# Optimization experiments

Measured on AMD Instinct MI355X. Metric: run time of the kernel, lower is better.

The kernel has to match this reference:

```python
import jax, jax.numpy as jnp
import numpy as np
from jax import lax

B, T, N, D = 8, 64, 197, 768
HID = 4
K_FRAME, K_TOKEN = 8, 49
LAMBDA_COV, LAMBDA_SCORE = 1.0, 0.5
LN_EPS = 1e-5


def setup_inputs() -> dict:
    key = jax.random.key(0)
    k = jax.random.split(key, 5)
    x = jax.random.normal(k[0], (B, T, N, D), jnp.float32)
    mask = jax.random.uniform(k[1], (B, T, N), jnp.float32)
    ln_gamma = jnp.ones((D,), jnp.float32)
    ln_beta = jnp.zeros((D,), jnp.float32)
    W1 = jax.random.normal(k[2], (D, HID * D), jnp.float32) * 0.02
    b1 = jnp.zeros((HID * D,), jnp.float32)
    W2 = jax.random.normal(k[3], (HID * D, 1), jnp.float32) * 0.02
    b2 = jnp.zeros((1,), jnp.float32)
    return {"x": x, "mask": mask, "ln_gamma": ln_gamma, "ln_beta": ln_beta,
            "W1": W1, "b1": b1, "W2": W2, "b2": b2}


def _facility_location(frame_repr, score, valid, k):
    # cosine similarity between frames (F.normalize eps = 1e-12)
    fn = frame_repr / jnp.clip(jnp.linalg.norm(frame_repr, axis=-1, keepdims=True), 1e-12)
    sim = jnp.einsum('bid,bjd->bij', fn, fn)  # [B,T,T]
    Bb, Tt = score.shape

    def step(carry, _):
        best_cover, chosen = carry  # [B,T], [B,T] bool
        # coverage gain per candidate j: sum_i max(best[i], sim[i,j]) - best[i]
        cov_gain = jnp.maximum(best_cover[:, :, None], sim).sum(1) - best_cover.sum(1, keepdims=True)
        total = LAMBDA_COV * cov_gain + LAMBDA_SCORE * score
        total = jnp.where(valid & (~chosen), total, -jnp.inf)
        j = jnp.argmax(total, axis=1)  # [B]
        sim_j = jnp.take_along_axis(sim, j[:, None, None], axis=2)[..., 0]  # [B,T]
        best_cover = jnp.maximum(best_cover, sim_j)
        chosen = chosen.at[jnp.arange(Bb), j].set(True)
        return (best_cover, chosen), j

    init = (jnp.zeros((Bb, Tt), frame_repr.dtype), jnp.zeros((Bb, Tt), bool))
    (_, chosen), js = lax.scan(step, init, None, length=k)
    return js.T, chosen.astype(frame_repr.dtype)  # frame_idx [B,k], frame_mask [B,T]


def _kcenter(X, valid, k):
    # X [N,D], valid [N] bool; greedy k-center (farthest point sampling)
    d0 = jnp.where(valid, (X * X).sum(-1), -jnp.inf)
    first = jnp.argmax(d0)

    def dist_to(i):
        diff = X - X[i]
        return jnp.sqrt((diff * diff).sum(-1))

    min_dist = jnp.where(valid, dist_to(first), -1.0)

    def step(md, _):
        cand = jnp.argmax(md)
        md = jnp.where(valid, jnp.minimum(md, dist_to(cand)), -1.0)
        return md, cand

    _, rest = lax.scan(step, min_dist, None, length=k - 1)
    return jnp.concatenate([first[None], rest])


def _forward(x, mask, ln_gamma, ln_beta, W1, b1, W2, b2):
    # masked mean frame representation (use_cls=False path)
    denom = jnp.clip(mask.sum(2), 1e-6)                      # [B,T]
    frame_repr = (x * mask[..., None]).sum(2) / denom[..., None]  # [B,T,D]
    valid_frame = denom > 0

    # score head: LayerNorm -> Linear -> GELU(exact) -> Linear
    mu = frame_repr.mean(-1, keepdims=True)
    var = ((frame_repr - mu) ** 2).mean(-1, keepdims=True)
    h = (frame_repr - mu) / jnp.sqrt(var + LN_EPS) * ln_gamma + ln_beta
    h = jax.nn.gelu(h @ W1 + b1, approximate=False)
    score = (h @ W2 + b2)[..., 0]                            # [B,T]

    # selection is index-valued: no gradient flows through it (as in torch)
    frame_idx, frame_mask = _facility_location(
        lax.stop_gradient(frame_repr), lax.stop_gradient(score), valid_frame, K_FRAME)

    Xf = jnp.take_along_axis(x, frame_idx[:, :, None, None], axis=1)   # [B,K,N,D]
    mf = jnp.take_along_axis(mask, frame_idx[:, :, None], axis=1) > 0.5  # [B,K,N]

    token_idx = jax.vmap(jax.vmap(lambda Xs, vs: _kcenter(Xs, vs, K_TOKEN)))(
        lax.stop_gradient(Xf), mf)                           # [B,K,Kt]

    b_ar = jnp.arange(x.shape[0])
    token_mask = jnp.zeros(mask.shape, x.dtype).at[
        b_ar[:, None, None], frame_idx[:, :, None], token_idx].set(1.0)

    z = jnp.take_along_axis(Xf, token_idx[..., None], axis=2)  # [B,K,Kt,D]
    return z, frame_idx, token_idx, frame_mask, token_mask


def reference(x, mask, ln_gamma, ln_beta, W1, b1, W2, b2):
    return _forward(x, mask, ln_gamma, ln_beta, W1, b1, W2, b2)
```

## Files before the change

### kernel.cpp

```cpp
#include <hip/hip_runtime.h>
#include <math.h>

#define B_ 8
#define T_ 64
#define N_ 197
#define D_ 768
#define HIDD_ 3072
#define KF_ 8
#define KT_ 49
#define GSTRIDE 200

#define Z_SZ    (B_*KF_*KT_*D_)
#define FI_OFF  (Z_SZ)
#define TI_OFF  (FI_OFF + B_*KF_)
#define FM_OFF  (TI_OFF + B_*KF_*KT_)
#define TM_OFF  (FM_OFF + B_*T_)
#define TM_SZ   (B_*T_*N_)

#define WS_SCOREP  0
#define WS_FN64    98304
#define WS_H32     (WS_FN64 + 3145728)
#define WS_VALID   (WS_H32 + 1572864)
#define WS_FIDX    (WS_VALID + 2048)
#define WS_SIM     (WS_FIDX + 256)
#define WS_G       (WS_SIM + 262144)

__global__ __launch_bounds__(256) void kA(const float* __restrict__ x,
                                          const float* __restrict__ mask,
                                          const float* __restrict__ gamma,
                                          const float* __restrict__ beta,
                                          double* __restrict__ fn64,
                                          float* __restrict__ h32,
                                          int* __restrict__ validw) {
  const int row = blockIdx.x;
  const int tid = threadIdx.x;
  __shared__ float  ms[N_];
  __shared__ double red[256];
  __shared__ double sh_denom, sh_mu, sh_sd, sh_nrm;
  const float* xr = x + (size_t)row * (N_ * D_);

  if (tid < N_) ms[tid] = mask[(size_t)row * N_ + tid];
  __syncthreads();

  red[tid] = (tid < N_) ? (double)ms[tid] : 0.0;
  __syncthreads();
  for (int s = 128; s > 0; s >>= 1) { if (tid < s) red[tid] += red[tid + s]; __syncthreads(); }
  if (tid == 0) { double d = red[0]; sh_denom = (d > 1e-6) ? d : 1e-6; }
  __syncthreads();
  const double dn = sh_denom;

  double a0 = 0.0, a1 = 0.0, a2 = 0.0, a3 = 0.0;
  if (tid < 192) {
    const float* px = xr + tid * 4;
#pragma unroll 4
    for (int n = 0; n < N_; n++) {
      const double mv = (double)ms[n];
      const float4 v = *(const float4*)(px + (size_t)n * D_);
      a0 += (double)v.x * mv;
      a1 += (double)v.y * mv;
      a2 += (double)v.z * mv;
      a3 += (double)v.w * mv;
    }
  }
  const double f0 = a0 / dn, f1 = a1 / dn, f2 = a2 / dn, f3 = a3 / dn;

  red[tid] = (tid < 192) ? (f0 + f1 + f2 + f3) : 0.0; __syncthreads();
  for (int s = 128; s > 0; s >>= 1) { if (tid < s) red[tid] += red[tid + s]; __syncthreads(); }
  if (tid == 0) sh_mu = red[0] / (double)D_;
  __syncthreads();
  const double mu = sh_mu;

  red[tid] = (tid < 192) ? (f0 * f0 + f1 * f1 + f2 * f2 + f3 * f3) : 0.0; __syncthreads();
  for (int s = 128; s > 0; s >>= 1) { if (tid < s) red[tid] += red[tid + s]; __syncthreads(); }
  if (tid == 0) { double nr = sqrt(red[0]); sh_nrm = (nr > 1e-12) ? nr : 1e-12; }
  __syncthreads();

  red[tid] = (tid < 192) ? ((f0 - mu) * (f0 - mu) + (f1 - mu) * (f1 - mu) +
                            (f2 - mu) * (f2 - mu) + (f3 - mu) * (f3 - mu)) : 0.0;
  __syncthreads();
  for (int s = 128; s > 0; s >>= 1) { if (tid < s) red[tid] += red[tid + s]; __syncthreads(); }
  if (tid == 0) sh_sd = sqrt(red[0] / (double)D_ + 1e-5);
  __syncthreads();
  const double sd = sh_sd, nrm = sh_nrm;

  if (tid < 192) {
    const size_t base = (size_t)row * D_;
    const float4 g  = ((const float4*)gamma)[tid];
    const float4 be = ((const float4*)beta)[tid];
    float4 hv;
    hv.x = (float)((f0 - mu) / sd * (double)g.x + (double)be.x);
    hv.y = (float)((f1 - mu) / sd * (double)g.y + (double)be.y);
    hv.z = (float)((f2 - mu) / sd * (double)g.z + (double)be.z);
    hv.w = (float)((f3 - mu) / sd * (double)g.w + (double)be.w);
    *(float4*)(h32 + base + tid * 4) = hv;
    double2* fp = (double2*)(fn64 + base + tid * 4);
    fp[0] = make_double2(f0 / nrm, f1 / nrm);
    fp[1] = make_double2(f2 / nrm, f3 / nrm);
  }
  if (tid == 0) validw[row] = 1;
}

__global__ __launch_bounds__(256) void kSB(const double* __restrict__ fn64,
                                           double* __restrict__ simG,
                                           const float* __restrict__ h32,
                                           const float* __restrict__ W1,
                                           const float* __restrict__ b1,
                                           const float* __restrict__ W2,
                                           double* __restrict__ scorep) {
  __shared__ char smem[42496] __attribute__((aligned(16)));
  const int tid = threadIdx.x;

  if (blockIdx.x < 32) {
    const int b    = blockIdx.x >> 2;
    const int tile = blockIdx.x & 3;
    const int ty = tid >> 4;
    const int tx = tid & 15;
    double* As = (double*)smem;
    double* Bs = (double*)(smem + 8704);
    double acc[4] = {0.0, 0.0, 0.0, 0.0};

    for (int kc = 0; kc < 12; kc++) {
#pragma unroll
      for (int it = 0; it < 4; it++) {
        const int idx = (it << 8) + tid;
        const int row = idx >> 6, kk = idx & 63;
        As[kk * 17 + row] = fn64[((size_t)(b * T_ + tile * 16 + row)) * D_ + kc * 64 + kk];
      }
#pragma unroll
      for (int it = 0; it < 16; it++) {
        const int idx = (it << 8) + tid;
        const int row = idx >> 6, kk = idx & 63;
        Bs[kk * 66 + row] = fn64[((size_t)(b * T_ + row)) * D_ + kc * 64 + kk];
      }
      __syncthreads();
#pragma unroll 8
      for (int kk = 0; kk < 64; kk++) {
        const double a = As[kk * 17 + ty];
        const double* bp = Bs + kk * 66 + tx * 4;
        acc[0] += a * bp[0];
        acc[1] += a * bp[1];
        acc[2] += a * bp[2];
        acc[3] += a * bp[3];
      }
      __syncthreads();
    }
    double* o = simG + ((size_t)b * 64 + tile * 16 + ty) * 64 + tx * 4;
    o[0] = acc[0]; o[1] = acc[1]; o[2] = acc[2]; o[3] = acc[3];
  } else {
    const int bid2 = blockIdx.x - 32;
    const int nb = bid2 % 24;
    const int n0 = nb * 128;
    const int m0 = (bid2 / 24) * 32;
    const int tx = tid & 31;
    const int ty = tid >> 5;
    float* As = (float*)smem;
    float* Bs = (float*)(smem + 9216);
    float acc[4][4];
#pragma unroll
    for (int r = 0; r < 4; r++)
#pragma unroll
      for (int c = 0; c < 4; c++) acc[r][c] = 0.0f;

    for (int kc = 0; kc < 12; kc++) {
      const int k0 = kc * 64;
#pragma unroll
      for (int it = 0; it < 8; it++) {
        int idx = tid + (it << 8);
        int k = idx & 63, m = idx >> 6;
        As[k * 36 + m] = h32[(size_t)(m0 + m) * D_ + k0 + k];
      }
#pragma unroll
      for (int it = 0; it < 8; it++) {
        int idx = tid + (it << 8);
        int k = idx >> 5, n4 = idx & 31;
        const float4 v = *(const float4*)(W1 + (size_t)(k0 + k) * HIDD_ + n0 + (n4 << 2));
        *(float4*)(Bs + k * 128 + (n4 << 2)) = v;
      }
      __syncthreads();
#pragma unroll 16
      for (int kk = 0; kk < 64; kk++) {
        float4 av = *(const float4*)(As + kk * 36 + ty * 4);
        float4 bv = *(const float4*)(Bs + kk * 128 + tx * 4);
        const float a[4] = {av.x, av.y, av.z, av.w};
        const float bb[4] = {bv.x, bv.y, bv.z, bv.w};
#pragma unroll
        for (int r = 0; r < 4; r++)
#pragma unroll
          for (int c = 0; c < 4; c++) acc[r][c] += a[r] * bb[c];
      }
      __syncthreads();
    }

    double part[4] = {0.0, 0.0, 0.0, 0.0};
#pragma unroll
    for (int r = 0; r < 4; r++) {
#pragma unroll
      for (int c = 0; c < 4; c++) {
        const int gn = n0 + tx * 4 + c;
        const double v = (double)(acc[r][c] + b1[gn]);
        const double g = 0.5 * v * (1.0 + erf(v * 0.7071067811865475244));
        part[r] += g * (double)W2[gn];
      }
    }
#pragma unroll
    for (int r = 0; r < 4; r++) {
      double s = part[r];
#pragma unroll
      for (int off = 16; off > 0; off >>= 1) s += __shfl_down(s, off, 32);
      if (tx == 0) scorep[(size_t)(m0 + ty * 4 + r) * 24 + nb] = s;
    }
  }
}

__global__ __launch_bounds__(256) void kD(const double* __restrict__ simG,
                                          const double* __restrict__ scorep,
                                          const float* __restrict__ b2,
                                          int* __restrict__ fidxw,
                                          float* __restrict__ out_fidx,
                                          float* __restrict__ out_fmask) {
  const int b = blockIdx.x;
  const int tid = threadIdx.x;
  __shared__ double sim[64 * 64];

  const double2* sp = (const double2*)(simG + (size_t)b * 4096);
#pragma unroll
  for (int it = 0; it < 8; it++) {
    const int idx = (it << 8) + tid;
    ((double2*)sim)[idx] = sp[idx];
  }
  __syncthreads();

  if (tid < 64) {
    double s = 0.0;
    const double* pp = scorep + (size_t)(b * T_ + tid) * 24;
    for (int q = 0; q < 24; q++) s += pp[q];
    const double half_score = 0.5 * (s + (double)b2[0]);

    double bc_r = 0.0;
    int chosen_r = 0;

    for (int step = 0; step < KF_; step++) {
      double gsum = 0.0;
      for (int ii = 0; ii < 64; ii++) {
        const double bcv = __shfl(bc_r, ii, 64);
        gsum += fmax(bcv, sim[ii * 64 + tid]);
      }
      double tot = gsum + half_score;
      if (chosen_r) tot = -INFINITY;

      double bv = tot; int bi = tid;
#pragma unroll
      for (int off = 1; off < 64; off <<= 1) {
        const double ov = __shfl_xor(bv, off, 64);
        const int    oi = __shfl_xor(bi, off, 64);
        if (ov > bv || (ov == bv && oi < bi)) { bv = ov; bi = oi; }
      }
      bc_r = fmax(bc_r, sim[bi * 64 + tid]);
      if (tid == bi) chosen_r = 1;
      if (tid == 0) {
        fidxw[b * KF_ + step] = bi;
        out_fidx[b * KF_ + step] = (float)bi;
      }
    }
    out_fmask[b * T_ + tid] = chosen_r ? 1.0f : 0.0f;
  }
}

__global__ __launch_bounds__(256) void kG(const float* __restrict__ x,
                                          const int* __restrict__ fidxw,
                                          double* __restrict__ G) {
  static const int TIa[10] = {0,0,0,0,1,1,1,2,2,3};
  static const int TJa[10] = {0,1,2,3,1,2,3,2,3,3};
  const int p  = blockIdx.x / 10;
  const int t  = blockIdx.x - p * 10;
  const int ti = TIa[t], tj = TJa[t];
  const int b  = p >> 3;
  const int fi = fidxw[p];
  const float* X = x + ((size_t)(b * T_ + fi)) * (N_ * D_);
  double* Gp = G + (size_t)p * (GSTRIDE * GSTRIDE);

  __shared__ float As[32 * 68];
  __shared__ float Bs[32 * 68];
  const int tid = threadIdx.x;
  const int tx = tid & 15;
  const int ty = tid >> 4;
  double acc[4][4];
#pragma unroll
  for (int r = 0; r < 4; r++)
#pragma unroll
    for (int c = 0; c < 4; c++) acc[r][c] = 0.0;

  for (int kc = 0; kc < 24; kc++) {
#pragma unroll
    for (int it = 0; it < 2; it++) {
      const int idx = (it << 8) + tid;
      const int row = idx >> 3;
      const int kg  = idx & 7;
      const int gra = ti * 64 + row, grb = tj * 64 + row;
      const int ra = (gra < N_) ? gra : (N_ - 1);
      const int rb = (grb < N_) ? grb : (N_ - 1);
      const float4 va = *(const float4*)(X + (size_t)ra * D_ + kc * 32 + kg * 4);
      const float4 vb = *(const float4*)(X + (size_t)rb * D_ + kc * 32 + kg * 4);
      As[(kg * 4 + 0) * 68 + row] = va.x;
      As[(kg * 4 + 1) * 68 + row] = va.y;
      As[(kg * 4 + 2) * 68 + row] = va.z;
      As[(kg * 4 + 3) * 68 + row] = va.w;
      Bs[(kg * 4 + 0) * 68 + row] = vb.x;
      Bs[(kg * 4 + 1) * 68 + row] = vb.y;
      Bs[(kg * 4 + 2) * 68 + row] = vb.z;
      Bs[(kg * 4 + 3) * 68 + row] = vb.w;
    }
    __syncthreads();
#pragma unroll 8
    for (int kk = 0; kk < 32; kk++) {
      const float4 av = *(const float4*)(As + kk * 68 + ty * 4);
      const float4 bv = *(const float4*)(Bs + kk * 68 + tx * 4);
      const double a[4]  = {(double)av.x, (double)av.y, (double)av.z, (double)av.w};
      const double bb[4] = {(double)bv.x, (double)bv.y, (double)bv.z, (double)bv.w};
#pragma unroll
      for (int r = 0; r < 4; r++)
#pragma unroll
        for (int c = 0; c < 4; c++) acc[r][c] += a[r] * bb[c];
    }
    __syncthreads();
  }

#pragma unroll
  for (int r = 0; r < 4; r++) {
    const int gi = ti * 64 + ty * 4 + r;
#pragma unroll
    for (int c = 0; c < 4; c++) {
      const int gj = tj * 64 + tx * 4 + c;
      if (gi < N_ && gj < N_) {
        Gp[(size_t)gi * GSTRIDE + gj] = acc[r][c];
        if (ti != tj) Gp[(size_t)gj * GSTRIDE + gi] = acc[r][c];
      }
    }
  }
}

__global__ __launch_bounds__(256) void kE2(const double* __restrict__ G,
                                           const float* __restrict__ mask,
                                           const int* __restrict__ fidxw,
                                           const float* __restrict__ x,
                                           float* __restrict__ out) {
  const int p = blockIdx.x;
  const int b = p >> 3;
  const int fi = fidxw[p];
  const double* Gp = G + (size_t)p * (GSTRIDE * GSTRIDE);
  const float* mrow = mask + (size_t)(b * T_ + fi) * N_;
  const float* X = x + ((size_t)(b * T_ + fi)) * (N_ * D_);
  const int tid = threadIdx.x;

  __shared__ int toksS[KT_];

  if (tid < 64) {
    const int l = tid;
    double gd[4]; int vld[4]; double md[4];
#pragma unroll
    for (int q = 0; q < 4; q++) {
      const int pt = l + 64 * q;
      const bool live = pt < N_;
      gd[q] = live ? Gp[(size_t)pt * GSTRIDE + pt] : 0.0;
      vld[q] = (live && (mrow[live ? pt : 0] > 0.5f)) ? 1 : 0;
      md[q] = -INFINITY;
    }

    double bv = vld[0] ? gd[0] : -INFINITY;
    int bi = l;
#pragma unroll
    for (int q = 1; q < 4; q++) {
      const double v = vld[q] ? gd[q] : -INFINITY;
      if (v > bv) { bv = v; bi = l + 64 * q; }
    }
#pragma unroll
    for (int off = 1; off < 64; off <<= 1) {
      const double ov = __shfl_xor(bv, off, 64);
      const int    oi = __shfl_xor(bi, off, 64);
      if (ov > bv || (ov == bv && oi < bi)) { bv = ov; bi = oi; }
    }
    int cand = bi;
    if (l == 0) toksS[0] = cand;

    for (int k = 1; k < KT_; k++) {
      const size_t rowbase = (size_t)cand * GSTRIDE;
      const double gdc = Gp[rowbase + cand];
      const double g0 = Gp[rowbase + l];
      const double g1 = Gp[rowbase + l + 64];
      const double g2 = Gp[rowbase + l + 128];
      const double d0 = sqrt(fmax(gd[0] + gdc - 2.0 * g0, 0.0));
      const double d1 = sqrt(fmax(gd[1] + gdc - 2.0 * g1, 0.0));
      const double d2 = sqrt(fmax(gd[2] + gdc - 2.0 * g2, 0.0));
      md[0] = vld[0] ? ((k == 1) ? d0 : fmin(md[0], d0)) : -1.0;
      md[1] = vld[1] ? ((k == 1) ? d1 : fmin(md[1], d1)) : -1.0;
      md[2] = vld[2] ? ((k == 1) ? d2 : fmin(md[2], d2)) : -1.0;
      if (l + 192 < N_) {
        const double g3 = Gp[rowbase + l + 192];
        const double d3 = sqrt(fmax(gd[3] + gdc - 2.0 * g3, 0.0));
        md[3] = vld[3] ? ((k == 1) ? d3 : fmin(md[3], d3)) : -1.0;
      }

      bv = md[0]; bi = l;
      if (md[1] > bv) { bv = md[1]; bi = l + 64; }
      if (md[2] > bv) { bv = md[2]; bi = l + 128; }
      if (md[3] > bv) { bv = md[3]; bi = l + 192; }
#pragma unroll
      for (int off = 1; off < 64; off <<= 1) {
        const double ov = __shfl_xor(bv, off, 64);
        const int    oi = __shfl_xor(bi, off, 64);
        if (ov > bv || (ov == bv && oi < bi)) { bv = ov; bi = oi; }
      }
      cand = bi;
      if (l == 0) toksS[k] = cand;
    }
  }
  __syncthreads();

  if (tid < KT_) {
    const int tok = toksS[tid];
    out[TI_OFF + p * KT_ + tid] = (float)tok;
    out[TM_OFF + (size_t)(b * T_ + fi) * N_ + tok] = 1.0f;
  }
  if (tid < 192) {
    for (int r = 0; r < KT_; r++) {
      const float4 v = *(const float4*)(X + (size_t)toksS[r] * D_ + tid * 4);
      *(float4*)(out + ((size_t)(p * KT_ + r)) * D_ + tid * 4) = v;
    }
  }
}

extern "C" void kernel_launch(void* const* d_in, const int* in_sizes, int n_in,
                              void* d_out, int out_size, void* d_ws, size_t ws_size,
                              hipStream_t stream) {
  (void)in_sizes; (void)n_in; (void)ws_size; (void)out_size;
  const float* x     = (const float*)d_in[0];
  const float* mask  = (const float*)d_in[1];
  const float* gamma = (const float*)d_in[2];
  const float* beta  = (const float*)d_in[3];
  const float* W1    = (const float*)d_in[4];
  const float* b1    = (const float*)d_in[5];
  const float* W2    = (const float*)d_in[6];
  const float* b2    = (const float*)d_in[7];
  float* out = (float*)d_out;
  char* ws = (char*)d_ws;

  double* scorep = (double*)(ws + WS_SCOREP);
  double* fn64   = (double*)(ws + WS_FN64);
  float*  h32    = (float*)(ws + WS_H32);
  int*    validw = (int*)(ws + WS_VALID);
  int*    fidxw  = (int*)(ws + WS_FIDX);
  double* simG   = (double*)(ws + WS_SIM);
  double* G      = (double*)(ws + WS_G);

  hipMemsetAsync(out + TM_OFF, 0, (size_t)TM_SZ * sizeof(float), stream);

  kA<<<B_ * T_, 256, 0, stream>>>(x, mask, gamma, beta, fn64, h32, validw);
  kSB<<<32 + (HIDD_ / 128) * ((B_ * T_) / 32), 256, 0, stream>>>(
      fn64, simG, h32, W1, b1, W2, scorep);
  kD<<<B_, 256, 0, stream>>>(simG, scorep, b2, fidxw, out + FI_OFF, out + FM_OFF);
  kG<<<B_ * KF_ * 10, 256, 0, stream>>>(x, fidxw, G);
  kE2<<<B_ * KF_, 256, 0, stream>>>(G, mask, fidxw, x, out);
}
```

Baseline: 744.7 us.

## Store Gram tiles as double in LDS, reuse A tile on diagonal, remap blocks per XCD

The Gram-matrix kernel now converts inputs to double once when staging into shared memory instead of on every inner-loop read. On diagonal tiles it reuses the A tile as B, skipping the second load. B columns are strided by 16 to cut bank conflicts, and block IDs are remapped so the tiles of one frame share an XCD for L2 locality. In the k-center loop the candidate's diagonal Gram value now comes from a wavefront shuffle instead of a global load. The cost is doubled LDS per block, which may reduce occupancy.

```diff
diff --git a/kernel.cpp b/kernel.cpp
--- a/kernel.cpp
+++ b/kernel.cpp
@@ -271,19 +271,24 @@
                                           double* __restrict__ G) {
   static const int TIa[10] = {0,0,0,0,1,1,1,2,2,3};
   static const int TJa[10] = {0,1,2,3,1,2,3,2,3,3};
-  const int p  = blockIdx.x / 10;
-  const int t  = blockIdx.x - p * 10;
+  const int bid  = blockIdx.x;
+  const int xcd  = bid & 7;
+  const int slot = bid >> 3;
+  const int p    = xcd + 8 * (slot / 10);
+  const int t    = slot % 10;
   const int ti = TIa[t], tj = TJa[t];
   const int b  = p >> 3;
   const int fi = fidxw[p];
   const float* X = x + ((size_t)(b * T_ + fi)) * (N_ * D_);
   double* Gp = G + (size_t)p * (GSTRIDE * GSTRIDE);
 
-  __shared__ float As[32 * 68];
-  __shared__ float Bs[32 * 68];
+  __shared__ double As[32 * 70];
+  __shared__ double Bs[32 * 70];
   const int tid = threadIdx.x;
   const int tx = tid & 15;
   const int ty = tid >> 4;
+  const bool diag = (ti == tj);
+  const double* Bsel = diag ? As : Bs;
   double acc[4][4];
 #pragma unroll
   for (int r = 0; r < 4; r++)
@@ -296,31 +301,34 @@
       const int idx = (it << 8) + tid;
       const int row = idx >> 3;
       const int kg  = idx & 7;
-      const int gra = ti * 64 + row, grb = tj * 64 + row;
+      const int gra = ti * 64 + row;
       const int ra = (gra < N_) ? gra : (N_ - 1);
-      const int rb = (grb < N_) ? grb : (N_ - 1);
       const float4 va = *(const float4*)(X + (size_t)ra * D_ + kc * 32 + kg * 4);
-      const float4 vb = *(const float4*)(X + (size_t)rb * D_ + kc * 32 + kg * 4);
-      As[(kg * 4 + 0) * 68 + row] = va.x;
-      As[(kg * 4 + 1) * 68 + row] = va.y;
-      As[(kg * 4 + 2) * 68 + row] = va.z;
-      As[(kg * 4 + 3) * 68 + row] = va.w;
-      Bs[(kg * 4 + 0) * 68 + row] = vb.x;
-      Bs[(kg * 4 + 1) * 68 + row] = vb.y;
-      Bs[(kg * 4 + 2) * 68 + row] = vb.z;
-      Bs[(kg * 4 + 3) * 68 + row] = vb.w;
+      As[(kg * 4 + 0) * 70 + row] = (double)va.x;
+      As[(kg * 4 + 1) * 70 + row] = (double)va.y;
+      As[(kg * 4 + 2) * 70 + row] = (double)va.z;
+      As[(kg * 4 + 3) * 70 + row] = (double)va.w;
+      if (!diag) {
+        const int grb = tj * 64 + row;
+        const int rb = (grb < N_) ? grb : (N_ - 1);
+        const float4 vb = *(const float4*)(X + (size_t)rb * D_ + kc * 32 + kg * 4);
+        Bs[(kg * 4 + 0) * 70 + row] = (double)vb.x;
+        Bs[(kg * 4 + 1) * 70 + row] = (double)vb.y;
+        Bs[(kg * 4 + 2) * 70 + row] = (double)vb.z;
+        Bs[(kg * 4 + 3) * 70 + row] = (double)vb.w;
+      }
     }
     __syncthreads();
 #pragma unroll 8
     for (int kk = 0; kk < 32; kk++) {
-      const float4 av = *(const float4*)(As + kk * 68 + ty * 4);
-      const float4 bv = *(const float4*)(Bs + kk * 68 + tx * 4);
-      const double a[4]  = {(double)av.x, (double)av.y, (double)av.z, (double)av.w};
-      const double bb[4] = {(double)bv.x, (double)bv.y, (double)bv.z, (double)bv.w};
-#pragma unroll
-      for (int r = 0; r < 4; r++)
-#pragma unroll
-        for (int c = 0; c < 4; c++) acc[r][c] += a[r] * bb[c];
+      const double* ap = As + kk * 70 + ty * 4;
+      const double a0 = ap[0], a1 = ap[1], a2 = ap[2], a3 = ap[3];
+      const double* bp = Bsel + kk * 70 + tx;
+      const double b0 = bp[0], b1 = bp[16], b2 = bp[32], b3 = bp[48];
+      acc[0][0] += a0 * b0; acc[0][1] += a0 * b1; acc[0][2] += a0 * b2; acc[0][3] += a0 * b3;
+      acc[1][0] += a1 * b0; acc[1][1] += a1 * b1; acc[1][2] += a1 * b2; acc[1][3] += a1 * b3;
+      acc[2][0] += a2 * b0; acc[2][1] += a2 * b1; acc[2][2] += a2 * b2; acc[2][3] += a2 * b3;
+      acc[3][0] += a3 * b0; acc[3][1] += a3 * b1; acc[3][2] += a3 * b2; acc[3][3] += a3 * b3;
     }
     __syncthreads();
   }
@@ -330,10 +338,10 @@
     const int gi = ti * 64 + ty * 4 + r;
 #pragma unroll
     for (int c = 0; c < 4; c++) {
-      const int gj = tj * 64 + tx * 4 + c;
+      const int gj = tj * 64 + c * 16 + tx;
       if (gi < N_ && gj < N_) {
         Gp[(size_t)gi * GSTRIDE + gj] = acc[r][c];
-        if (ti != tj) Gp[(size_t)gj * GSTRIDE + gi] = acc[r][c];
+        if (!diag) Gp[(size_t)gj * GSTRIDE + gi] = acc[r][c];
       }
     }
   }
@@ -384,10 +392,13 @@
 
     for (int k = 1; k < KT_; k++) {
       const size_t rowbase = (size_t)cand * GSTRIDE;
-      const double gdc = Gp[rowbase + cand];
       const double g0 = Gp[rowbase + l];
       const double g1 = Gp[rowbase + l + 64];
       const double g2 = Gp[rowbase + l + 128];
+      const int cq = cand >> 6, cl = cand & 63;
+      const double gsel = (cq == 0) ? gd[0] : (cq == 1) ? gd[1]
+                        : (cq == 2) ? gd[2] : gd[3];
+      const double gdc = __shfl(gsel, cl, 64);
       const double d0 = sqrt(fmax(gd[0] + gdc - 2.0 * g0, 0.0));
       const double d1 = sqrt(fmax(gd[1] + gdc - 2.0 * g1, 0.0));
       const double d2 = sqrt(fmax(gd[2] + gdc - 2.0 * g2, 0.0));
```

New measurement: 758.1 us. No clear change (+1.8%).
